# Optimization experiments

Measured on AMD Instinct MI355X. Metric: run time of the kernel, lower is better.

## Reference

```python
import jax, jax.numpy as jnp
import numpy as np

N_NODES = 50000


def _sage_conv(x, src, dst, Wl, bl, Wr):
    # mean aggregation of source-node features into target nodes
    agg = jax.ops.segment_sum(x[src], dst, num_segments=N_NODES)      # [N, C]
    deg = jax.ops.segment_sum(jnp.ones_like(src, dtype=x.dtype), dst,
                              num_segments=N_NODES)                   # [N]
    mean = agg / jnp.maximum(deg, 1.0)[:, None]
    # PyG SAGEConv: lin_l(aggr) (with bias) + lin_r(x) (no bias)
    return mean @ Wl.T + bl + x @ Wr.T


def setup_inputs() -> dict:
    key = jax.random.key(0)
    ks = jax.random.split(key, 8)
    C = 128
    E = 600000
    scale = 1.0 / np.sqrt(C)
    x = jax.random.normal(ks[0], (N_NODES, C), dtype=jnp.float32)
    edge_index = jax.random.randint(ks[1], (2, E), 0, N_NODES, dtype=jnp.int64)
    Wl1 = jax.random.normal(ks[2], (C, C), dtype=jnp.float32) * scale
    bl1 = jnp.zeros((C,), dtype=jnp.float32)
    Wr1 = jax.random.normal(ks[3], (C, C), dtype=jnp.float32) * scale
    Wl2 = jax.random.normal(ks[4], (C, C), dtype=jnp.float32) * scale
    bl2 = jnp.zeros((C,), dtype=jnp.float32)
    Wr2 = jax.random.normal(ks[5], (C, C), dtype=jnp.float32) * scale
    return {"x": x, "edge_index": edge_index, "Wl1": Wl1, "bl1": bl1,
            "Wr1": Wr1, "Wl2": Wl2, "bl2": bl2, "Wr2": Wr2}


def reference(x, edge_index, Wl1, bl1, Wr1, Wl2, bl2, Wr2):
    src, dst = edge_index[0], edge_index[1]
    h = _sage_conv(x, src, dst, Wl1, bl1, Wr1)
    h = jax.nn.relu(h)
    out = _sage_conv(h, src, dst, Wl2, bl2, Wr2)
    return out
```

## Files before the change

### kernel.cpp

```cpp
#include <hip/hip_runtime.h>
#include <hip/hip_bf16.h>

#define N_NODES 50000
#define C 128
#define NPAD 50176
#define NTILES (NPAD / 16)
#define GEMM_BLOCKS (NTILES / 8)
#define XPREP_BLOCKS 3125
#define WPREP_BLOCKS 256
#define CAP 48
#define EPT 4

typedef short bf16x8 __attribute__((ext_vector_type(8)));
typedef float f32x4 __attribute__((ext_vector_type(4)));

__device__ __forceinline__ unsigned short f2bf(float f) {
    unsigned int u = __float_as_uint(f);
    unsigned int r = u + 0x7fffu + ((u >> 16) & 1u);
    return (unsigned short)(r >> 16);
}

__device__ __forceinline__ float bf2f(unsigned short b) {
    return __uint_as_float(((unsigned int)b) << 16);
}

__device__ __forceinline__ void acc8(float* a, uint4 u) {
    const unsigned int uu[4] = {u.x, u.y, u.z, u.w};
#pragma unroll
    for (int i = 0; i < 4; ++i) {
        a[2 * i] += bf2f((unsigned short)uu[i]);
        a[2 * i + 1] += bf2f((unsigned short)(uu[i] >> 16));
    }
}

__global__ __launch_bounds__(256) void buildfill_kernel(
    const int* __restrict__ src, const int* __restrict__ dst, int E, int edgeBlocks,
    int* __restrict__ cursor, int* __restrict__ csr,
    const float* __restrict__ x, unsigned short* __restrict__ Xb,
    const float* __restrict__ Wl1, const float* __restrict__ Wr1,
    const float* __restrict__ Wl2, const float* __restrict__ Wr2,
    unsigned short* __restrict__ Wc1, unsigned short* __restrict__ Wc2) {
    int b = blockIdx.x;
    if (b < edgeBlocks) {
        int e0 = b * (256 * EPT) + threadIdx.x;
        int dd[EPT], ss[EPT], slot[EPT];
        bool val[EPT];
#pragma unroll
        for (int k = 0; k < EPT; ++k) {
            int e = e0 + k * 256;
            val[k] = e < E;
            if (val[k]) {
                dd[k] = dst[e];
                ss[k] = src[e];
                val[k] = ((unsigned)dd[k] < (unsigned)N_NODES) &&
                         ((unsigned)ss[k] < (unsigned)N_NODES);
            }
        }
#pragma unroll
        for (int k = 0; k < EPT; ++k)
            if (val[k]) slot[k] = atomicAdd(cursor + dd[k], 1);
#pragma unroll
        for (int k = 0; k < EPT; ++k)
            if (val[k] && slot[k] < CAP) csr[dd[k] * CAP + slot[k]] = ss[k];
    } else if (b < edgeBlocks + XPREP_BLOCKS) {
        int t = (b - edgeBlocks) * 256 + threadIdx.x;
        if (t >= N_NODES * C / 8) return;
        const float4 a = *(const float4*)(x + (size_t)t * 8);
        const float4 c = *(const float4*)(x + (size_t)t * 8 + 4);
        unsigned short o[8] = {f2bf(a.x), f2bf(a.y), f2bf(a.z), f2bf(a.w),
                               f2bf(c.x), f2bf(c.y), f2bf(c.z), f2bf(c.w)};
        *(uint4*)(Xb + (size_t)t * 8) = *(const uint4*)o;
    } else {
        int idx = (b - edgeBlocks - XPREP_BLOCKS) * 256 + threadIdx.x;
        int layer = idx >> 15;
        int r = idx & 32767;
        int j = r >> 8, k = r & 255;
        const float* Wl = layer ? Wl2 : Wl1;
        const float* Wr = layer ? Wr2 : Wr1;
        unsigned short* Wc = layer ? Wc2 : Wc1;
        float f = (k < 128) ? Wl[j * 128 + k] : Wr[j * 128 + (k - 128)];
        Wc[r] = f2bf(f);
    }
}

__global__ __launch_bounds__(256) void gather_kernel(
    const unsigned short* __restrict__ feat,
    const int* __restrict__ cursor, const int* __restrict__ csr,
    unsigned short* __restrict__ Fm) {
    int w = (blockIdx.x * 256 + threadIdx.x) >> 6;
    int lane = threadIdx.x & 63;
    if (w >= N_NODES) return;
    const int deg = min(cursor[w], CAP);
    const int g = lane >> 4;
    const int c = lane & 15;
    float a[8];
#pragma unroll
    for (int i = 0; i < 8; ++i) a[i] = 0.f;
    int myidx = (lane < deg) ? csr[w * CAP + lane] : 0;
    const unsigned short* fp = feat + c * 8;
    int j = 0;
    for (; j + 8 <= deg; j += 8) {
        int s0 = __shfl(myidx, j + g);
        int s1 = __shfl(myidx, j + 4 + g);
        const uint4 u0 = *(const uint4*)(fp + (size_t)s0 * C);
        const uint4 u1 = *(const uint4*)(fp + (size_t)s1 * C);
        acc8(a, u0);
        acc8(a, u1);
    }
    if (j + 4 <= deg) {
        int s0 = __shfl(myidx, j + g);
        const uint4 u0 = *(const uint4*)(fp + (size_t)s0 * C);
        acc8(a, u0);
        j += 4;
    }
    int rem = deg - j;
    if (rem) {
        int s0 = __shfl(myidx, j + ((g < rem) ? g : 0));
        if (g < rem) {
            const uint4 u0 = *(const uint4*)(fp + (size_t)s0 * C);
            acc8(a, u0);
        }
    }
#pragma unroll
    for (int i = 0; i < 8; ++i) {
        a[i] += __shfl_xor(a[i], 16);
        a[i] += __shfl_xor(a[i], 32);
    }
    const float inv = 1.0f / fmaxf((float)deg, 1.0f);
    if (g == 0) {
        unsigned int o[4];
#pragma unroll
        for (int i = 0; i < 4; ++i)
            o[i] = (unsigned)f2bf(a[2 * i] * inv) |
                   ((unsigned)f2bf(a[2 * i + 1] * inv) << 16);
        *(uint4*)(Fm + (size_t)w * C + c * 8) = *(const uint4*)o;
    }
}

__global__ __launch_bounds__(256) void sage_gemm(
    const unsigned short* __restrict__ Fm,
    const unsigned short* __restrict__ Self,
    const unsigned short* __restrict__ Wc,
    const float* __restrict__ bias,
    void* __restrict__ outv, int relu, int obf16) {
    __shared__ unsigned short wl[128 * 264];
    for (int cidx = threadIdx.x; cidx < 4096; cidx += 256) {
        int row = cidx >> 5, chunk = cidx & 31;
        const uint4 v = *(const uint4*)(Wc + row * 256 + chunk * 8);
        *(uint4*)(&wl[row * 264 + chunk * 8]) = v;
    }
    __syncthreads();

    const int wave = threadIdx.x >> 6;
    const int lane = threadIdx.x & 63;
    const int m = lane & 15;
    const int q = lane >> 4;
    const int tile0 = blockIdx.x * 8 + wave * 2;

    const size_t rowoff = (size_t)(tile0 * 16 + m) * C + q * 8;
    const unsigned short* am = Fm + rowoff;
    const unsigned short* as = Self + rowoff;

    f32x4 acc[2][8];
#pragma unroll
    for (int t = 0; t < 2; ++t)
#pragma unroll
        for (int j = 0; j < 8; ++j) acc[t][j] = (f32x4){0.f, 0.f, 0.f, 0.f};

#pragma unroll
    for (int kt = 0; kt < 8; ++kt) {
        const unsigned short* A = (kt < 4) ? am : as;
        const int ko = (kt & 3) * 32;
        bf16x8 af0 = *(const bf16x8*)(A + ko);
        bf16x8 af1 = *(const bf16x8*)(A + 16 * C + ko);
#pragma unroll
        for (int jt = 0; jt < 8; ++jt) {
            bf16x8 bfrag = *(const bf16x8*)(&wl[(jt * 16 + m) * 264 + kt * 32 + q * 8]);
            acc[0][jt] = __builtin_amdgcn_mfma_f32_16x16x32_bf16(af0, bfrag, acc[0][jt], 0, 0, 0);
            acc[1][jt] = __builtin_amdgcn_mfma_f32_16x16x32_bf16(af1, bfrag, acc[1][jt], 0, 0, 0);
        }
    }

#pragma unroll
    for (int t = 0; t < 2; ++t) {
        int rbase = (tile0 + t) * 16 + q * 4;
#pragma unroll
        for (int r = 0; r < 4; ++r) {
            int row = rbase + r;
            if (row < N_NODES) {
#pragma unroll
                for (int jt = 0; jt < 8; ++jt) {
                    int col = jt * 16 + m;
                    float v = acc[t][jt][r] + bias[col];
                    if (relu) v = fmaxf(v, 0.0f);
                    if (obf16)
                        ((unsigned short*)outv)[(size_t)row * C + col] = f2bf(v);
                    else
                        ((float*)outv)[(size_t)row * C + col] = v;
                }
            }
        }
    }
}

extern "C" void kernel_launch(void* const* d_in, const int* in_sizes, int n_in,
                              void* d_out, int out_size, void* d_ws, size_t ws_size,
                              hipStream_t stream) {
    const float* x = (const float*)d_in[0];
    const int* edge = (const int*)d_in[1];
    const float* Wl1 = (const float*)d_in[2];
    const float* bl1 = (const float*)d_in[3];
    const float* Wr1 = (const float*)d_in[4];
    const float* Wl2 = (const float*)d_in[5];
    const float* bl2 = (const float*)d_in[6];
    const float* Wr2 = (const float*)d_in[7];
    float* out = (float*)d_out;

    const int E = in_sizes[1] / 2;
    const int* src = edge;
    const int* dst = edge + E;

    char* ws = (char*)d_ws;
    size_t off = 0;
    int* cursor = (int*)(ws + off);           off += (size_t)N_NODES * 4;
    off = (off + 511) & ~511ull;
    int* csr = (int*)(ws + off);              off += (size_t)N_NODES * CAP * 4;
    off = (off + 511) & ~511ull;
    unsigned short* Xb = (unsigned short*)(ws + off); off += (size_t)NPAD * C * 2;
    unsigned short* Fm = (unsigned short*)(ws + off); off += (size_t)NPAD * C * 2;
    unsigned short* h  = (unsigned short*)(ws + off); off += (size_t)NPAD * C * 2;
    unsigned short* Wc1 = (unsigned short*)(ws + off); off += 128 * 256 * 2;
    unsigned short* Wc2 = (unsigned short*)(ws + off); off += 128 * 256 * 2;
    (void)ws_size;

    const int edgeBlocks = (E + 256 * EPT - 1) / (256 * EPT);
    const int gatherBlocks = (NPAD * 64) / 256;

    hipMemsetAsync(cursor, 0, (size_t)N_NODES * 4, stream);
    buildfill_kernel<<<edgeBlocks + XPREP_BLOCKS + WPREP_BLOCKS, 256, 0, stream>>>(
        src, dst, E, edgeBlocks, cursor, csr, x, Xb, Wl1, Wr1, Wl2, Wr2, Wc1, Wc2);

    gather_kernel<<<gatherBlocks, 256, 0, stream>>>(Xb, cursor, csr, Fm);
    sage_gemm<<<GEMM_BLOCKS, 256, 0, stream>>>(Fm, Xb, Wc1, bl1, h, 1, 1);

    gather_kernel<<<gatherBlocks, 256, 0, stream>>>(h, cursor, csr, Fm);
    sage_gemm<<<GEMM_BLOCKS, 256, 0, stream>>>(Fm, h, Wc2, bl2, out, 0, 0);
}
```

Before: 223.2 us.

## Pad degree counters to separate cache lines and batch neighbor loads in gather

```diff
diff --git a/kernel.cpp b/kernel.cpp
--- a/kernel.cpp
+++ b/kernel.cpp
@@ -9,7 +9,7 @@
 #define XPREP_BLOCKS 3125
 #define WPREP_BLOCKS 256
 #define CAP 48
-#define EPT 4
+#define CSTRIDE 32
 
 typedef short bf16x8 __attribute__((ext_vector_type(8)));
 typedef float f32x4 __attribute__((ext_vector_type(4)));
@@ -42,26 +42,15 @@
     unsigned short* __restrict__ Wc1, unsigned short* __restrict__ Wc2) {
     int b = blockIdx.x;
     if (b < edgeBlocks) {
-        int e0 = b * (256 * EPT) + threadIdx.x;
-        int dd[EPT], ss[EPT], slot[EPT];
-        bool val[EPT];
-#pragma unroll
-        for (int k = 0; k < EPT; ++k) {
-            int e = e0 + k * 256;
-            val[k] = e < E;
-            if (val[k]) {
-                dd[k] = dst[e];
-                ss[k] = src[e];
-                val[k] = ((unsigned)dd[k] < (unsigned)N_NODES) &&
-                         ((unsigned)ss[k] < (unsigned)N_NODES);
+        int e = b * 256 + threadIdx.x;
+        if (e < E) {
+            int d = dst[e];
+            int s = src[e];
+            if ((unsigned)d < (unsigned)N_NODES && (unsigned)s < (unsigned)N_NODES) {
+                int slot = atomicAdd(cursor + d * CSTRIDE, 1);
+                if (slot < CAP) csr[d * CAP + slot] = s;
             }
         }
-#pragma unroll
-        for (int k = 0; k < EPT; ++k)
-            if (val[k]) slot[k] = atomicAdd(cursor + dd[k], 1);
-#pragma unroll
-        for (int k = 0; k < EPT; ++k)
-            if (val[k] && slot[k] < CAP) csr[dd[k] * CAP + slot[k]] = ss[k];
     } else if (b < edgeBlocks + XPREP_BLOCKS) {
         int t = (b - edgeBlocks) * 256 + threadIdx.x;
         if (t >= N_NODES * C / 8) return;
@@ -90,35 +79,37 @@
     int w = (blockIdx.x * 256 + threadIdx.x) >> 6;
     int lane = threadIdx.x & 63;
     if (w >= N_NODES) return;
-    const int deg = min(cursor[w], CAP);
     const int g = lane >> 4;
     const int c = lane & 15;
+    const int degraw = cursor[(size_t)w * CSTRIDE];
+    const int myidx = (lane < CAP) ? csr[w * CAP + lane] : 0;
+    const int deg = min(degraw, CAP);
     float a[8];
 #pragma unroll
     for (int i = 0; i < 8; ++i) a[i] = 0.f;
-    int myidx = (lane < deg) ? csr[w * CAP + lane] : 0;
     const unsigned short* fp = feat + c * 8;
-    int j = 0;
-    for (; j + 8 <= deg; j += 8) {
-        int s0 = __shfl(myidx, j + g);
-        int s1 = __shfl(myidx, j + 4 + g);
-        const uint4 u0 = *(const uint4*)(fp + (size_t)s0 * C);
-        const uint4 u1 = *(const uint4*)(fp + (size_t)s1 * C);
-        acc8(a, u0);
-        acc8(a, u1);
-    }
-    if (j + 4 <= deg) {
-        int s0 = __shfl(myidx, j + g);
-        const uint4 u0 = *(const uint4*)(fp + (size_t)s0 * C);
-        acc8(a, u0);
-        j += 4;
-    }
-    int rem = deg - j;
-    if (rem) {
-        int s0 = __shfl(myidx, j + ((g < rem) ? g : 0));
-        if (g < rem) {
-            const uint4 u0 = *(const uint4*)(fp + (size_t)s0 * C);
-            acc8(a, u0);
+    const int nb = (deg + 3) >> 2;
+    uint4 u[6];
+#pragma unroll
+    for (int b = 0; b < 6; ++b) {
+        if (b < nb) {
+            int r = 4 * b + g;
+            int s = __shfl(myidx, r < deg ? r : 0);
+            u[b] = *(const uint4*)(fp + (size_t)s * C);
+        }
+    }
+#pragma unroll
+    for (int b = 0; b < 6; ++b) {
+        if (b < nb) {
+            if (4 * b + g < deg) acc8(a, u[b]);
+        }
+    }
+    if (nb > 6) {
+        for (int b = 6; b < nb; ++b) {
+            int r = 4 * b + g;
+            int s = __shfl(myidx, r < deg ? r : 0);
+            uint4 uu = *(const uint4*)(fp + (size_t)s * C);
+            if (r < deg) acc8(a, uu);
         }
     }
 #pragma unroll
@@ -222,7 +213,7 @@
 
     char* ws = (char*)d_ws;
     size_t off = 0;
-    int* cursor = (int*)(ws + off);           off += (size_t)N_NODES * 4;
+    int* cursor = (int*)(ws + off);           off += (size_t)N_NODES * CSTRIDE * 4;
     off = (off + 511) & ~511ull;
     int* csr = (int*)(ws + off);              off += (size_t)N_NODES * CAP * 4;
     off = (off + 511) & ~511ull;
@@ -233,10 +224,10 @@
     unsigned short* Wc2 = (unsigned short*)(ws + off); off += 128 * 256 * 2;
     (void)ws_size;
 
-    const int edgeBlocks = (E + 256 * EPT - 1) / (256 * EPT);
+    const int edgeBlocks = (E + 255) / 256;
     const int gatherBlocks = (NPAD * 64) / 256;
 
-    hipMemsetAsync(cursor, 0, (size_t)N_NODES * 4, stream);
+    hipMemsetAsync(cursor, 0, (size_t)N_NODES * CSTRIDE * 4, stream);
     buildfill_kernel<<<edgeBlocks + XPREP_BLOCKS + WPREP_BLOCKS, 256, 0, stream>>>(
         src, dst, E, edgeBlocks, cursor, csr, x, Xb, Wl1, Wr1, Wl2, Wr2, Wc1, Wc2);
 
```

Result: faster. 208.7 us (-6.5%).
